# Kernel optimization log

Measured on AMD Instinct MI355X. Metric: run time of the kernel, lower is better.

The kernel has to match this reference:

```python
import jax, jax.numpy as jnp
import numpy as np

WIN = (8, 8)
HEADS = 6
DIM = 192
N_TOK = WIN[0] * WIN[1]


def _cpb_coords_table():
    # (2*Wh-1, 2*Ww-1, 2) log-spaced continuous relative coords, flattened to (T, 2)
    h = np.arange(-(WIN[0] - 1), WIN[0], dtype=np.float32)
    w = np.arange(-(WIN[1] - 1), WIN[1], dtype=np.float32)
    t = np.stack(np.meshgrid(h, w, indexing='ij'), axis=-1)
    t[..., 0] /= WIN[0] - 1
    t[..., 1] /= WIN[1] - 1
    t *= 8.0
    t = np.sign(t) * np.log2(np.abs(t) + 1.0) / np.log2(8.0)
    return jnp.asarray(t.reshape(-1, 2))


def _rel_pos_index():
    ch, cw = np.meshgrid(np.arange(WIN[0]), np.arange(WIN[1]), indexing='ij')
    cf = np.stack([ch.ravel(), cw.ravel()])  # (2, N)
    rc = (cf[:, :, None] - cf[:, None, :]).transpose(1, 2, 0)  # (N, N, 2)
    rc[..., 0] += WIN[0] - 1
    rc[..., 1] += WIN[1] - 1
    rc[..., 0] *= 2 * WIN[1] - 1
    return jnp.asarray(rc.sum(-1).ravel())  # (N*N,)


_COORDS = _cpb_coords_table()
_RPI = _rel_pos_index()


def setup_inputs() -> dict:
    key = jax.random.key(0)
    ks = jax.random.split(key, 8)
    B_ = 4096
    x = jax.random.normal(ks[0], (B_, N_TOK, DIM), dtype=jnp.float32)
    mask = jnp.zeros((64, N_TOK, N_TOK), dtype=jnp.float32)
    qkv_w = jax.random.normal(ks[1], (3 * DIM, DIM), dtype=jnp.float32) * 0.02
    q_bias = jnp.zeros((DIM,), dtype=jnp.float32)
    v_bias = jnp.zeros((DIM,), dtype=jnp.float32)
    logit_scale = jnp.log(10.0) * jnp.ones((HEADS, 1, 1), dtype=jnp.float32)
    cpb_w1 = jax.random.normal(ks[2], (512, 2), dtype=jnp.float32) * 0.02
    cpb_b1 = jnp.zeros((512,), dtype=jnp.float32)
    cpb_w2 = jax.random.normal(ks[3], (HEADS, 512), dtype=jnp.float32) * 0.02
    proj_w = jax.random.normal(ks[4], (DIM, DIM), dtype=jnp.float32) * 0.02
    proj_b = jnp.zeros((DIM,), dtype=jnp.float32)
    return {"x": x, "mask": mask, "qkv_w": qkv_w, "q_bias": q_bias, "v_bias": v_bias,
            "logit_scale": logit_scale, "cpb_w1": cpb_w1, "cpb_b1": cpb_b1,
            "cpb_w2": cpb_w2, "proj_w": proj_w, "proj_b": proj_b}


def reference(x, mask, qkv_w, q_bias, v_bias, logit_scale, cpb_w1, cpb_b1, cpb_w2, proj_w, proj_b):
    B, N, C = x.shape
    H = HEADS
    d = C // H
    # qkv projection; bias layout matches torch.stack((q_bias, 0, v_bias)).view(3*C)
    qkv_bias = jnp.concatenate([q_bias, jnp.zeros_like(v_bias), v_bias])
    qkv = (x @ qkv_w.T + qkv_bias).reshape(B, N, 3, H, d).transpose(2, 0, 3, 1, 4)
    q, k, v = qkv[0], qkv[1], qkv[2]  # (B, H, N, d)
    # cosine attention: L2-normalize q, k (F.normalize with eps=1e-12)
    qn = q / jnp.maximum(jnp.linalg.norm(q, axis=-1, keepdims=True), 1e-12)
    kn = k / jnp.maximum(jnp.linalg.norm(k, axis=-1, keepdims=True), 1e-12)
    attn = jnp.einsum('bhnd,bhmd->bhnm', qn, kn)
    scale = jnp.exp(jnp.minimum(logit_scale, jnp.log(100.0)))  # clamp at 1/0.01
    attn = attn * scale  # (H,1,1) broadcasts over (B,H,N,N)
    # continuous position bias: MLP(2->512->H) on log-coords, gathered per pair
    tbl = jax.nn.relu(_COORDS @ cpb_w1.T + cpb_b1) @ cpb_w2.T  # (T, H)
    rpb = tbl[_RPI].reshape(N, N, H).transpose(2, 0, 1)  # (H, N, N)
    attn = attn + 16.0 * jax.nn.sigmoid(rpb)[None]
    nW = mask.shape[0]
    attn = attn.reshape(B // nW, nW, H, N, N) + mask[None, :, None]
    attn = jax.nn.softmax(attn.reshape(B, H, N, N), axis=-1)
    out = jnp.einsum('bhnm,bhmd->bhnd', attn, v).transpose(0, 2, 1, 3).reshape(B, N, C)
    return out @ proj_w.T + proj_b
```

## Files before the change

### kernel.cpp

```cpp
#include <hip/hip_runtime.h>
#include <math.h>

typedef __bf16 bf16_t;
typedef __bf16 bf16x8_t __attribute__((ext_vector_type(8)));
typedef __bf16 bf16x4_t __attribute__((ext_vector_type(4)));
typedef float f32x4_t __attribute__((ext_vector_type(4)));

#define MFMA(a, b, c) __builtin_amdgcn_mfma_f32_16x16x32_bf16((a), (b), (c), 0, 0, 0)

#define WS_WQKV 0u
#define WS_WPROJ 221184u
#define WS_QBIAS 294912u
#define WS_SCALE 297216u
#define WS_TBL 297472u
#define WS_BIAS16 303104u

__global__ __launch_bounds__(64) void cpb_table_kernel(
    const float* __restrict__ w1, const float* __restrict__ b1,
    const float* __restrict__ w2, float* __restrict__ tbl) {
  int t = blockIdx.x;
  int lane = threadIdx.x;
  int dh = t / 15 - 7, dw = t % 15 - 7;
  float th = (float)dh * (8.0f / 7.0f);
  float tw = (float)dw * (8.0f / 7.0f);
  float c0 = copysignf(log2f(fabsf(th) + 1.0f) / 3.0f, th);
  float c1 = copysignf(log2f(fabsf(tw) + 1.0f) / 3.0f, tw);
  float acc[6] = {0.f, 0.f, 0.f, 0.f, 0.f, 0.f};
  for (int k = lane; k < 512; k += 64) {
    float hv = fmaxf(w1[2 * k] * c0 + w1[2 * k + 1] * c1 + b1[k], 0.0f);
#pragma unroll
    for (int hh = 0; hh < 6; ++hh) acc[hh] += hv * w2[hh * 512 + k];
  }
#pragma unroll
  for (int hh = 0; hh < 6; ++hh) {
#pragma unroll
    for (int m = 1; m < 64; m <<= 1) acc[hh] += __shfl_xor(acc[hh], m, 64);
  }
  if (lane == 0) {
#pragma unroll
    for (int hh = 0; hh < 6; ++hh) tbl[t * 6 + hh] = acc[hh];
  }
}

__global__ __launch_bounds__(256) void prep_kernel(
    const float* __restrict__ qkv_w, const float* __restrict__ proj_w,
    const float* __restrict__ q_bias, const float* __restrict__ v_bias,
    const float* __restrict__ logit_scale, const float* __restrict__ tbl,
    bf16_t* __restrict__ wqkv, bf16_t* __restrict__ wproj,
    float* __restrict__ qbias, float* __restrict__ scalev,
    float* __restrict__ bias16) {
  int id = blockIdx.x * 256 + threadIdx.x;
  if (id < 110592) {
    wqkv[id] = (bf16_t)qkv_w[id];
  } else if (id < 147456) {
    int i = id - 110592;
    wproj[i] = (bf16_t)proj_w[i];
  } else if (id < 148032) {
    int i = id - 147456;
    float bv = (i < 192) ? q_bias[i] : ((i < 384) ? 0.0f : v_bias[i - 384]);
    qbias[i] = bv;
  } else if (id < 148038) {
    int hh = id - 148032;
    scalev[hh] = expf(fminf(logit_scale[hh], logf(100.0f)));
  } else if (id < 172614) {
    int i = id - 148038;
    int hh = i >> 12;
    int nm = i & 4095;
    int n = nm >> 6, m = nm & 63;
    int i1 = n >> 3, j1 = n & 7, i2 = m >> 3, j2 = m & 7;
    int rpi = (i1 - i2 + 7) * 15 + (j1 - j2 + 7);
    float v = tbl[rpi * 6 + hh];
    bias16[i] = 16.0f / (1.0f + __expf(-v));
  }
}

__global__ __launch_bounds__(768) void wattn_kernel(
    const float* __restrict__ x, const float* __restrict__ mask,
    const bf16_t* __restrict__ wqkv, const bf16_t* __restrict__ wproj,
    const float* __restrict__ qbias, const float* __restrict__ scalev,
    const float* __restrict__ bias16, const float* __restrict__ proj_b,
    float* __restrict__ out, int nw) {
  __shared__ __align__(16) char smem[131072];
  bf16_t* xs = (bf16_t*)smem;
  bf16_t* qs = (bf16_t*)(smem + 25600);
  bf16_t* Ps = (bf16_t*)smem;
  bf16_t* ksv = (bf16_t*)(smem + 56320);
  bf16_t* os = (bf16_t*)(smem + 56320);
  bf16_t* vts = (bf16_t*)(smem + 87040);
  float* msk = (float*)(smem + 114688);

  const int tid = threadIdx.x;
  const int wave = tid >> 6, lane = tid & 63;
  const int h = wave >> 1, s = wave & 1;
  const int quad = lane >> 4, col = lane & 15;
  const int b = blockIdx.x;

  const float4* xg = (const float4*)(x + (size_t)b * 12288);
  for (int i = tid; i < 3072; i += 768) {
    float4 v = xg[i];
    int row = i / 48;
    int c = (i - row * 48) * 4;
    bf16x4_t pk = {(bf16_t)v.x, (bf16_t)v.y, (bf16_t)v.z, (bf16_t)v.w};
    *(bf16x4_t*)(xs + row * 200 + c) = pk;
  }
  const float* mg = mask + (size_t)(b % nw) * 4096;
  for (int i = tid; i < 4096; i += 768) msk[i] = mg[i];
  __syncthreads();

  const float sc_h = scalev[h];
  const int mrow0 = 32 * s + col;
  const int mrow1 = mrow0 + 16;
  const int koff = quad * 8;
  const f32x4_t zz = {0.f, 0.f, 0.f, 0.f};

  for (int g = 0; g < 3; ++g) {
    int nbase = g * 192 + h * 32;
    f32x4_t a00 = zz, a01 = zz, a10 = zz, a11 = zz;
#pragma unroll
    for (int kk = 0; kk < 6; ++kk) {
      int k0 = kk * 32 + koff;
      bf16x8_t fa0 = *(const bf16x8_t*)(xs + mrow0 * 200 + k0);
      bf16x8_t fa1 = *(const bf16x8_t*)(xs + mrow1 * 200 + k0);
      bf16x8_t fb0 = *(const bf16x8_t*)(wqkv + (size_t)(nbase + col) * 192 + k0);
      bf16x8_t fb1 = *(const bf16x8_t*)(wqkv + (size_t)(nbase + 16 + col) * 192 + k0);
      a00 = MFMA(fa0, fb0, a00);
      a01 = MFMA(fa0, fb1, a01);
      a10 = MFMA(fa1, fb0, a10);
      a11 = MFMA(fa1, fb1, a11);
    }
    float bn0 = qbias[nbase + col];
    float bn1 = qbias[nbase + 16 + col];
    if (g < 2) {
      float mult = (g == 0) ? sc_h : 1.0f;
      bf16_t* dst = ((g == 0) ? qs : ksv) + h * 2560;
#pragma unroll
      for (int mi2 = 0; mi2 < 2; ++mi2) {
        f32x4_t va = mi2 ? a10 : a00;
        f32x4_t vb = mi2 ? a11 : a01;
#pragma unroll
        for (int r = 0; r < 4; ++r) {
          float v0 = va[r] + bn0, v1 = vb[r] + bn1;
          float ss = v0 * v0 + v1 * v1;
          ss += __shfl_xor(ss, 1, 64);
          ss += __shfl_xor(ss, 2, 64);
          ss += __shfl_xor(ss, 4, 64);
          ss += __shfl_xor(ss, 8, 64);
          float inv = mult / fmaxf(sqrtf(ss), 1e-12f);
          int token = (2 * s + mi2) * 16 + quad * 4 + r;
          dst[token * 40 + col] = (bf16_t)(v0 * inv);
          dst[token * 40 + 16 + col] = (bf16_t)(v1 * inv);
        }
      }
    } else {
      bf16_t* dst = vts + h * 2304;
#pragma unroll
      for (int mi2 = 0; mi2 < 2; ++mi2) {
        f32x4_t va = mi2 ? a10 : a00;
        f32x4_t vb = mi2 ? a11 : a01;
#pragma unroll
        for (int r = 0; r < 4; ++r) {
          int token = (2 * s + mi2) * 16 + quad * 4 + r;
          dst[col * 72 + token] = (bf16_t)(va[r] + bn0);
          dst[(16 + col) * 72 + token] = (bf16_t)(vb[r] + bn1);
        }
      }
    }
  }
  __syncthreads();

  f32x4_t at[2][4];
  {
    const bf16_t* qh = qs + h * 2560;
    const bf16_t* kh = ksv + h * 2560;
    bf16x8_t aq0 = *(const bf16x8_t*)(qh + mrow0 * 40 + koff);
    bf16x8_t aq1 = *(const bf16x8_t*)(qh + mrow1 * 40 + koff);
#pragma unroll
    for (int ni = 0; ni < 4; ++ni) {
      bf16x8_t bk = *(const bf16x8_t*)(kh + (ni * 16 + col) * 40 + koff);
      at[0][ni] = MFMA(aq0, bk, zz);
      at[1][ni] = MFMA(aq1, bk, zz);
    }
  }

  float p[2][4][4];
  const float* bg = bias16 + h * 4096;
#pragma unroll
  for (int mi2 = 0; mi2 < 2; ++mi2) {
#pragma unroll
    for (int r = 0; r < 4; ++r) {
      int m = (2 * s + mi2) * 16 + quad * 4 + r;
      float vals[4];
#pragma unroll
      for (int ni = 0; ni < 4; ++ni) {
        int n = ni * 16 + col;
        vals[ni] = at[mi2][ni][r] + bg[m * 64 + n] + msk[m * 64 + n];
      }
      float mx = fmaxf(fmaxf(vals[0], vals[1]), fmaxf(vals[2], vals[3]));
      mx = fmaxf(mx, __shfl_xor(mx, 1, 64));
      mx = fmaxf(mx, __shfl_xor(mx, 2, 64));
      mx = fmaxf(mx, __shfl_xor(mx, 4, 64));
      mx = fmaxf(mx, __shfl_xor(mx, 8, 64));
      float sm = 0.f;
#pragma unroll
      for (int ni = 0; ni < 4; ++ni) {
        vals[ni] = __expf(vals[ni] - mx);
        sm += vals[ni];
      }
      sm += __shfl_xor(sm, 1, 64);
      sm += __shfl_xor(sm, 2, 64);
      sm += __shfl_xor(sm, 4, 64);
      sm += __shfl_xor(sm, 8, 64);
      float inv = 1.0f / sm;
#pragma unroll
      for (int ni = 0; ni < 4; ++ni) p[mi2][ni][r] = vals[ni] * inv;
    }
  }
  __syncthreads();

  bf16_t* Ph = Ps + h * 4608;
#pragma unroll
  for (int mi2 = 0; mi2 < 2; ++mi2) {
#pragma unroll
    for (int ni = 0; ni < 4; ++ni) {
#pragma unroll
      for (int r = 0; r < 4; ++r) {
        int m = (2 * s + mi2) * 16 + quad * 4 + r;
        Ph[m * 72 + ni * 16 + col] = (bf16_t)p[mi2][ni][r];
      }
    }
  }

  f32x4_t oac[2][2] = {{zz, zz}, {zz, zz}};
  {
    const bf16_t* vh = vts + h * 2304;
#pragma unroll
    for (int kk = 0; kk < 2; ++kk) {
      int k0 = kk * 32 + koff;
      bf16x8_t pa0 = *(const bf16x8_t*)(Ph + mrow0 * 72 + k0);
      bf16x8_t pa1 = *(const bf16x8_t*)(Ph + mrow1 * 72 + k0);
      bf16x8_t vb0 = *(const bf16x8_t*)(vh + col * 72 + k0);
      bf16x8_t vb1 = *(const bf16x8_t*)(vh + (16 + col) * 72 + k0);
      oac[0][0] = MFMA(pa0, vb0, oac[0][0]);
      oac[0][1] = MFMA(pa0, vb1, oac[0][1]);
      oac[1][0] = MFMA(pa1, vb0, oac[1][0]);
      oac[1][1] = MFMA(pa1, vb1, oac[1][1]);
    }
  }
#pragma unroll
  for (int mi2 = 0; mi2 < 2; ++mi2) {
#pragma unroll
    for (int ni = 0; ni < 2; ++ni) {
#pragma unroll
      for (int r = 0; r < 4; ++r) {
        int token = (2 * s + mi2) * 16 + quad * 4 + r;
        os[token * 200 + h * 32 + ni * 16 + col] = (bf16_t)oac[mi2][ni][r];
      }
    }
  }
  __syncthreads();

  f32x4_t pr[2][2] = {{zz, zz}, {zz, zz}};
#pragma unroll
  for (int kk = 0; kk < 6; ++kk) {
    int k0 = kk * 32 + koff;
    bf16x8_t fa0 = *(const bf16x8_t*)(os + mrow0 * 200 + k0);
    bf16x8_t fa1 = *(const bf16x8_t*)(os + mrow1 * 200 + k0);
    bf16x8_t fb0 = *(const bf16x8_t*)(wproj + (size_t)(h * 32 + col) * 192 + k0);
    bf16x8_t fb1 = *(const bf16x8_t*)(wproj + (size_t)(h * 32 + 16 + col) * 192 + k0);
    pr[0][0] = MFMA(fa0, fb0, pr[0][0]);
    pr[0][1] = MFMA(fa0, fb1, pr[0][1]);
    pr[1][0] = MFMA(fa1, fb0, pr[1][0]);
    pr[1][1] = MFMA(fa1, fb1, pr[1][1]);
  }
  float pb0 = proj_b[h * 32 + col];
  float pb1 = proj_b[h * 32 + 16 + col];
  float* og = out + (size_t)b * 12288;
#pragma unroll
  for (int mi2 = 0; mi2 < 2; ++mi2) {
#pragma unroll
    for (int r = 0; r < 4; ++r) {
      int token = (2 * s + mi2) * 16 + quad * 4 + r;
      og[token * 192 + h * 32 + col] = pr[mi2][0][r] + pb0;
      og[token * 192 + h * 32 + 16 + col] = pr[mi2][1][r] + pb1;
    }
  }
}

extern "C" void kernel_launch(void* const* d_in, const int* in_sizes, int n_in,
                              void* d_out, int out_size, void* d_ws, size_t ws_size,
                              hipStream_t stream) {
  const float* x = (const float*)d_in[0];
  const float* mask = (const float*)d_in[1];
  const float* qkv_w = (const float*)d_in[2];
  const float* q_bias = (const float*)d_in[3];
  const float* v_bias = (const float*)d_in[4];
  const float* logit_scale = (const float*)d_in[5];
  const float* cpb_w1 = (const float*)d_in[6];
  const float* cpb_b1 = (const float*)d_in[7];
  const float* cpb_w2 = (const float*)d_in[8];
  const float* proj_w = (const float*)d_in[9];
  const float* proj_b = (const float*)d_in[10];
  float* out = (float*)d_out;

  char* ws = (char*)d_ws;
  bf16_t* wqkv = (bf16_t*)(ws + WS_WQKV);
  bf16_t* wproj = (bf16_t*)(ws + WS_WPROJ);
  float* qbias = (float*)(ws + WS_QBIAS);
  float* scalev = (float*)(ws + WS_SCALE);
  float* tbl = (float*)(ws + WS_TBL);
  float* bias16 = (float*)(ws + WS_BIAS16);

  const int nwin = in_sizes[0] / 12288;
  const int nw = in_sizes[1] / 4096;

  cpb_table_kernel<<<dim3(225), dim3(64), 0, stream>>>(cpb_w1, cpb_b1, cpb_w2, tbl);
  prep_kernel<<<dim3(675), dim3(256), 0, stream>>>(qkv_w, proj_w, q_bias, v_bias,
                                                   logit_scale, tbl, wqkv, wproj,
                                                   qbias, scalev, bias16);
  wattn_kernel<<<dim3(nwin), dim3(768), 0, stream>>>(x, mask, wqkv, wproj, qbias,
                                                     scalev, bias16, proj_b, out, nw);
}
```

Measured before the change: 704.2 us.

## Shrink shared memory by aliasing buffers and reading mask from global

Reorganizes the shared memory layout from 128 KB to about 77 KB. Q is now kept in registers and written over the x buffer, K is stored in a token-major layout, and P overwrites the x/Q region. The mask is no longer staged in LDS but read directly from global memory. The x load is vectorized to four float4 per thread, and launch_bounds is given a min-blocks hint. The goal is to lower LDS use so two 768-thread blocks can fit per CU. In exchange it adds an extra barrier and uncached global mask reads.

```diff
diff --git a/kernel.cpp b/kernel.cpp
--- a/kernel.cpp
+++ b/kernel.cpp
@@ -74,20 +74,18 @@
   }
 }
 
-__global__ __launch_bounds__(768) void wattn_kernel(
+__global__ __launch_bounds__(768, 6) void wattn_kernel(
     const float* __restrict__ x, const float* __restrict__ mask,
     const bf16_t* __restrict__ wqkv, const bf16_t* __restrict__ wproj,
     const float* __restrict__ qbias, const float* __restrict__ scalev,
     const float* __restrict__ bias16, const float* __restrict__ proj_b,
     float* __restrict__ out, int nw) {
-  __shared__ __align__(16) char smem[131072];
+  __shared__ __align__(16) char smem[78848];
   bf16_t* xs = (bf16_t*)smem;
-  bf16_t* qs = (bf16_t*)(smem + 25600);
+  bf16_t* ksv = (bf16_t*)(smem + 25600);
+  bf16_t* vts = (bf16_t*)(smem + 51200);
   bf16_t* Ps = (bf16_t*)smem;
-  bf16_t* ksv = (bf16_t*)(smem + 56320);
-  bf16_t* os = (bf16_t*)(smem + 56320);
-  bf16_t* vts = (bf16_t*)(smem + 87040);
-  float* msk = (float*)(smem + 114688);
+  bf16_t* os = (bf16_t*)(smem + 51200);
 
   const int tid = threadIdx.x;
   const int wave = tid >> 6, lane = tid & 63;
@@ -95,16 +93,21 @@
   const int quad = lane >> 4, col = lane & 15;
   const int b = blockIdx.x;
 
-  const float4* xg = (const float4*)(x + (size_t)b * 12288);
-  for (int i = tid; i < 3072; i += 768) {
-    float4 v = xg[i];
-    int row = i / 48;
-    int c = (i - row * 48) * 4;
-    bf16x4_t pk = {(bf16_t)v.x, (bf16_t)v.y, (bf16_t)v.z, (bf16_t)v.w};
-    *(bf16x4_t*)(xs + row * 200 + c) = pk;
-  }
-  const float* mg = mask + (size_t)(b % nw) * 4096;
-  for (int i = tid; i < 4096; i += 768) msk[i] = mg[i];
+  {
+    const float4* xg = (const float4*)(x + (size_t)b * 12288);
+    float4 v0 = xg[4 * tid + 0];
+    float4 v1 = xg[4 * tid + 1];
+    float4 v2 = xg[4 * tid + 2];
+    float4 v3 = xg[4 * tid + 3];
+    int row = tid / 12;
+    int cc = (tid % 12) * 16;
+    bf16x8_t p0 = {(bf16_t)v0.x, (bf16_t)v0.y, (bf16_t)v0.z, (bf16_t)v0.w,
+                   (bf16_t)v1.x, (bf16_t)v1.y, (bf16_t)v1.z, (bf16_t)v1.w};
+    bf16x8_t p1 = {(bf16_t)v2.x, (bf16_t)v2.y, (bf16_t)v2.z, (bf16_t)v2.w,
+                   (bf16_t)v3.x, (bf16_t)v3.y, (bf16_t)v3.z, (bf16_t)v3.w};
+    *(bf16x8_t*)(xs + row * 200 + cc) = p0;
+    *(bf16x8_t*)(xs + row * 200 + cc + 8) = p1;
+  }
   __syncthreads();
 
   const float sc_h = scalev[h];
@@ -113,8 +116,12 @@
   const int koff = quad * 8;
   const f32x4_t zz = {0.f, 0.f, 0.f, 0.f};
 
-  for (int g = 0; g < 3; ++g) {
-    int nbase = g * 192 + h * 32;
+  bf16_t qreg[2][2][4];
+
+#pragma unroll
+  for (int gi = 0; gi < 3; ++gi) {
+    const int g = (gi == 0) ? 1 : ((gi == 1) ? 2 : 0);
+    const int nbase = g * 192 + h * 32;
     f32x4_t a00 = zz, a01 = zz, a10 = zz, a11 = zz;
 #pragma unroll
     for (int kk = 0; kk < 6; ++kk) {
@@ -130,9 +137,20 @@
     }
     float bn0 = qbias[nbase + col];
     float bn1 = qbias[nbase + 16 + col];
-    if (g < 2) {
+    if (g == 2) {
+#pragma unroll
+      for (int mi2 = 0; mi2 < 2; ++mi2) {
+        f32x4_t va = mi2 ? a10 : a00;
+        f32x4_t vb = mi2 ? a11 : a01;
+#pragma unroll
+        for (int r = 0; r < 4; ++r) {
+          int token = (2 * s + mi2) * 16 + quad * 4 + r;
+          vts[(h * 32 + col) * 72 + token] = (bf16_t)(va[r] + bn0);
+          vts[(h * 32 + 16 + col) * 72 + token] = (bf16_t)(vb[r] + bn1);
+        }
+      }
+    } else {
       float mult = (g == 0) ? sc_h : 1.0f;
-      bf16_t* dst = ((g == 0) ? qs : ksv) + h * 2560;
 #pragma unroll
       for (int mi2 = 0; mi2 < 2; ++mi2) {
         f32x4_t va = mi2 ? a10 : a00;
@@ -146,37 +164,38 @@
           ss += __shfl_xor(ss, 4, 64);
           ss += __shfl_xor(ss, 8, 64);
           float inv = mult / fmaxf(sqrtf(ss), 1e-12f);
-          int token = (2 * s + mi2) * 16 + quad * 4 + r;
-          dst[token * 40 + col] = (bf16_t)(v0 * inv);
-          dst[token * 40 + 16 + col] = (bf16_t)(v1 * inv);
+          if (g == 1) {
+            int token = (2 * s + mi2) * 16 + quad * 4 + r;
+            ksv[token * 200 + h * 32 + col] = (bf16_t)(v0 * inv);
+            ksv[token * 200 + h * 32 + 16 + col] = (bf16_t)(v1 * inv);
+          } else {
+            qreg[mi2][0][r] = (bf16_t)(v0 * inv);
+            qreg[mi2][1][r] = (bf16_t)(v1 * inv);
+          }
         }
       }
-    } else {
-      bf16_t* dst = vts + h * 2304;
-#pragma unroll
-      for (int mi2 = 0; mi2 < 2; ++mi2) {
-        f32x4_t va = mi2 ? a10 : a00;
-        f32x4_t vb = mi2 ? a11 : a01;
-#pragma unroll
-        for (int r = 0; r < 4; ++r) {
-          int token = (2 * s + mi2) * 16 + quad * 4 + r;
-          dst[col * 72 + token] = (bf16_t)(va[r] + bn0);
-          dst[(16 + col) * 72 + token] = (bf16_t)(vb[r] + bn1);
-        }
-      }
-    }
-  }
-  __syncthreads();
+    }
+  }
+  __syncthreads();
+
+  bf16_t* Qs = xs;
+#pragma unroll
+  for (int mi2 = 0; mi2 < 2; ++mi2) {
+#pragma unroll
+    for (int r = 0; r < 4; ++r) {
+      int token = (2 * s + mi2) * 16 + quad * 4 + r;
+      Qs[token * 200 + h * 32 + col] = qreg[mi2][0][r];
+      Qs[token * 200 + h * 32 + 16 + col] = qreg[mi2][1][r];
+    }
+  }
 
   f32x4_t at[2][4];
   {
-    const bf16_t* qh = qs + h * 2560;
-    const bf16_t* kh = ksv + h * 2560;
-    bf16x8_t aq0 = *(const bf16x8_t*)(qh + mrow0 * 40 + koff);
-    bf16x8_t aq1 = *(const bf16x8_t*)(qh + mrow1 * 40 + koff);
+    bf16x8_t aq0 = *(const bf16x8_t*)(Qs + mrow0 * 200 + h * 32 + koff);
+    bf16x8_t aq1 = *(const bf16x8_t*)(Qs + mrow1 * 200 + h * 32 + koff);
 #pragma unroll
     for (int ni = 0; ni < 4; ++ni) {
-      bf16x8_t bk = *(const bf16x8_t*)(kh + (ni * 16 + col) * 40 + koff);
+      bf16x8_t bk = *(const bf16x8_t*)(ksv + (ni * 16 + col) * 200 + h * 32 + koff);
       at[0][ni] = MFMA(aq0, bk, zz);
       at[1][ni] = MFMA(aq1, bk, zz);
     }
@@ -184,6 +203,7 @@
 
   float p[2][4][4];
   const float* bg = bias16 + h * 4096;
+  const float* mg = mask + (size_t)(b % nw) * 4096;
 #pragma unroll
   for (int mi2 = 0; mi2 < 2; ++mi2) {
 #pragma unroll
@@ -193,7 +213,7 @@
 #pragma unroll
       for (int ni = 0; ni < 4; ++ni) {
         int n = ni * 16 + col;
-        vals[ni] = at[mi2][ni][r] + bg[m * 64 + n] + msk[m * 64 + n];
+        vals[ni] = at[mi2][ni][r] + bg[m * 64 + n] + mg[m * 64 + n];
       }
       float mx = fmaxf(fmaxf(vals[0], vals[1]), fmaxf(vals[2], vals[3]));
       mx = fmaxf(mx, __shfl_xor(mx, 1, 64));
@@ -217,7 +237,6 @@
   }
   __syncthreads();
 
-  bf16_t* Ph = Ps + h * 4608;
 #pragma unroll
   for (int mi2 = 0; mi2 < 2; ++mi2) {
 #pragma unroll
@@ -225,27 +244,26 @@
 #pragma unroll
       for (int r = 0; r < 4; ++r) {
         int m = (2 * s + mi2) * 16 + quad * 4 + r;
-        Ph[m * 72 + ni * 16 + col] = (bf16_t)p[mi2][ni][r];
+        Ps[m * 392 + h * 64 + ni * 16 + col] = (bf16_t)p[mi2][ni][r];
       }
     }
   }
 
   f32x4_t oac[2][2] = {{zz, zz}, {zz, zz}};
-  {
-    const bf16_t* vh = vts + h * 2304;
-#pragma unroll
-    for (int kk = 0; kk < 2; ++kk) {
-      int k0 = kk * 32 + koff;
-      bf16x8_t pa0 = *(const bf16x8_t*)(Ph + mrow0 * 72 + k0);
-      bf16x8_t pa1 = *(const bf16x8_t*)(Ph + mrow1 * 72 + k0);
-      bf16x8_t vb0 = *(const bf16x8_t*)(vh + col * 72 + k0);
-      bf16x8_t vb1 = *(const bf16x8_t*)(vh + (16 + col) * 72 + k0);
-      oac[0][0] = MFMA(pa0, vb0, oac[0][0]);
-      oac[0][1] = MFMA(pa0, vb1, oac[0][1]);
-      oac[1][0] = MFMA(pa1, vb0, oac[1][0]);
-      oac[1][1] = MFMA(pa1, vb1, oac[1][1]);
-    }
-  }
+#pragma unroll
+  for (int kk = 0; kk < 2; ++kk) {
+    int k0 = kk * 32 + koff;
+    bf16x8_t pa0 = *(const bf16x8_t*)(Ps + mrow0 * 392 + h * 64 + k0);
+    bf16x8_t pa1 = *(const bf16x8_t*)(Ps + mrow1 * 392 + h * 64 + k0);
+    bf16x8_t vb0 = *(const bf16x8_t*)(vts + (h * 32 + col) * 72 + k0);
+    bf16x8_t vb1 = *(const bf16x8_t*)(vts + (h * 32 + 16 + col) * 72 + k0);
+    oac[0][0] = MFMA(pa0, vb0, oac[0][0]);
+    oac[0][1] = MFMA(pa0, vb1, oac[0][1]);
+    oac[1][0] = MFMA(pa1, vb0, oac[1][0]);
+    oac[1][1] = MFMA(pa1, vb1, oac[1][1]);
+  }
+  __syncthreads();
+
 #pragma unroll
   for (int mi2 = 0; mi2 < 2; ++mi2) {
 #pragma unroll
```

Result: slower. 756.5 us (+7.4%).
